# Optimization experiments

Hardware: AMD Instinct MI355X
Metric: run time of the kernel (lower is better)

## Reference

```python
import jax, jax.numpy as jnp
import numpy as np

B, T, D, L, VOCAB = 4, 2048, 512, 3, 256


def setup_inputs() -> dict:
    key = jax.random.key(0)
    ks = jax.random.split(key, 5)
    x = jax.random.randint(ks[0], (B, T), 0, VOCAB, dtype=jnp.int32)
    embed = jax.random.normal(ks[1], (VOCAB, D), dtype=jnp.float32) * 0.02
    k = jnp.ones((L,), dtype=jnp.float32)
    ln_gamma = jnp.ones((L, D), dtype=jnp.float32)
    ln_beta = jnp.zeros((L, D), dtype=jnp.float32)
    W1 = jax.random.normal(ks[2], (L, D, 4 * D), dtype=jnp.float32) * 0.02
    b1 = jnp.zeros((L, 4 * D), dtype=jnp.float32)
    W2 = jax.random.normal(ks[3], (L, 4 * D, D), dtype=jnp.float32) * 0.02
    b2 = jnp.zeros((L, D), dtype=jnp.float32)
    return {"x": x, "embed": embed, "k": k, "ln_gamma": ln_gamma,
            "ln_beta": ln_beta, "W1": W1, "b1": b1, "W2": W2, "b2": b2}


def _layernorm(x, g, b, eps=1e-3):  # keras default eps=1e-3
    mu = jnp.mean(x, axis=-1, keepdims=True)
    var = jnp.mean(jnp.square(x - mu), axis=-1, keepdims=True)
    return (x - mu) * jax.lax.rsqrt(var + eps) * g + b


def reference(x, embed, k, ln_gamma, ln_beta, W1, b1, W2, b2):
    h = embed[x]  # (B,T,D)
    # CumprodBoundaryDimension: cumprod over feature dim, tanh, cumsum over time
    bd = jnp.cumsum(jnp.tanh(jnp.cumprod(h, axis=-1)), axis=1)
    h = h + h * bd
    t = jnp.arange(T)
    dist = jnp.abs((t[:, None] - t[None, :]).astype(jnp.float32))  # (T,T)
    causal = (t[None, :] <= t[:, None]).astype(jnp.float32)
    for l in range(L):
        # DeltaImportance
        h_cum = jnp.cumsum(h, axis=1)
        h_prev = jnp.pad(h[:, :-1, :], ((0, 0), (1, 0), (0, 0)))
        mag = jnp.linalg.norm(h_cum - h_prev, axis=-1)  # (B,T)
        decay = jnp.exp(-jax.nn.softplus(k[l]) * dist) * causal  # (T,T)
        # importance[b,i,j] = mag[b,i]*decay[i,j]; context = importance @ h
        ctx = jnp.abs(mag[:, :, None] * jnp.einsum('ij,bjd->bid', decay, h))
        y = _layernorm(ctx, ln_gamma[l], ln_beta[l])
        y = jax.nn.gelu(y @ W1[l] + b1[l], approximate=False) @ W2[l] + b2[l]
        h = h + y
    return h @ embed.T  # tied output projection (B,T,VOCAB)
```

## Files before the change

### kernel.cpp

```cpp
#include <hip/hip_runtime.h>
#include <math.h>


constexpr int Bc = 4, Tc = 2048, Dc = 512, Hc = 2048, Vc = 256;
constexpr int TSF = 16, NCF = 128;

typedef __attribute__((ext_vector_type(8))) short short8;
typedef __attribute__((ext_vector_type(4))) float f32x4;

__device__ inline unsigned short f2bf(float f) {
  unsigned int u = __float_as_uint(f);
  u += 0x7fffu + ((u >> 16) & 1u);
  return (unsigned short)(u >> 16);
}

__device__ inline void gload_lds16(const void* g, void* l) {
  __builtin_amdgcn_global_load_lds(
      (const __attribute__((address_space(1))) void*)g,
      (__attribute__((address_space(3))) void*)l, 16, 0, 0);
}

__device__ inline void wvm_dyn(int n) {
  switch (n) {
    case 14: asm volatile("s_waitcnt vmcnt(14)" ::: "memory"); break;
    case 12: asm volatile("s_waitcnt vmcnt(12)" ::: "memory"); break;
    case 10: asm volatile("s_waitcnt vmcnt(10)" ::: "memory"); break;
    case 8:  asm volatile("s_waitcnt vmcnt(8)"  ::: "memory"); break;
    case 6:  asm volatile("s_waitcnt vmcnt(6)"  ::: "memory"); break;
    case 4:  asm volatile("s_waitcnt vmcnt(4)"  ::: "memory"); break;
    case 2:  asm volatile("s_waitcnt vmcnt(2)"  ::: "memory"); break;
    default: asm volatile("s_waitcnt vmcnt(0)"  ::: "memory"); break;
  }
}
__device__ inline void barrier_raw() {
  asm volatile("s_barrier" ::: "memory");
}

__device__ inline float gelu_f(float z) {
  float x = z * 0.707106781186547524f;
  float ax = fabsf(x);
  float t = __builtin_amdgcn_rcpf(fmaf(0.3275911f, ax, 1.0f));
  float poly = t*(0.254829592f + t*(-0.284496736f + t*(1.421413741f +
               t*(-1.453152027f + t*1.061405429f))));
  float er = 1.0f - poly * __expf(-ax*ax);
  er = copysignf(er, x);
  return 0.5f * z * (1.0f + er);
}

__device__ inline float decay_w(const float* kvec, int l) {
  float kk = kvec[l];
  float sp = kk > 0.f ? kk + log1pf(expf(-kk)) : log1pf(expf(kk));
  return expf(-sp);
}

__device__ inline void tr32(const float* Wl, unsigned short* Wtl,
                            int R, int C, int c0, int r0, int tid,
                            float (*tile)[33]) {
  int tx = tid & 31, ty = tid >> 5;
  for (int i = ty; i < 32; i += 8)
    tile[i][tx] = Wl[(size_t)(r0+i)*C + (c0+tx)];
  __syncthreads();
  int rx = tid & 7, ry = tid >> 3;
  ushort4 o;
  o.x = f2bf(tile[rx*4+0][ry]);
  o.y = f2bf(tile[rx*4+1][ry]);
  o.z = f2bf(tile[rx*4+2][ry]);
  o.w = f2bf(tile[rx*4+3][ry]);
  *(ushort4*)&Wtl[(size_t)(c0+ry)*R + (r0 + rx*4)] = o;
}

__global__ __launch_bounds__(256) void wprep(
    const float* __restrict__ W1, unsigned short* __restrict__ W1t,
    const float* __restrict__ W2, unsigned short* __restrict__ W2t,
    const float* __restrict__ embed, unsigned short* __restrict__ emb)
{
  __shared__ float tile[32][33];
  int bid = blockIdx.x, tid = threadIdx.x;
  if (bid < 3072) {
    int l = bid >> 10, rem = bid & 1023;
    int cx = rem & 63, ry = rem >> 6;
    tr32(W1 + (size_t)l*Dc*Hc, W1t + (size_t)l*Dc*Hc, Dc, Hc,
         cx*32, ry*32, tid, tile);
  } else if (bid < 6144) {
    int b2 = bid - 3072;
    int l = b2 >> 10, rem = b2 & 1023;
    int cx = rem & 15, ry = rem >> 4;
    tr32(W2 + (size_t)l*Hc*Dc, W2t + (size_t)l*Hc*Dc, Hc, Dc,
         cx*32, ry*32, tid, tile);
  } else {
    int i = ((bid - 6144)*256 + tid) * 4;
    if (i < Vc*Dc) {
      float4 v = *(const float4*)&embed[i];
      ushort4 o;
      o.x = f2bf(v.x); o.y = f2bf(v.y); o.z = f2bf(v.z); o.w = f2bf(v.w);
      *(ushort4*)&emb[i] = o;
    }
  }
}

__global__ __launch_bounds__(1024) void embed_part(
    const int* __restrict__ x, const float* __restrict__ embed,
    float* __restrict__ th, float* __restrict__ partA)
{
  int c = blockIdx.x, b = blockIdx.y;
  int wv = threadIdx.x >> 6, lane = threadIdx.x & 63;
  int token = b*Tc + c*TSF + wv;
  int row = x[token];
  const float* e = embed + (size_t)row * Dc + lane * 8;
  float v[8];
  {
    float4 a = *(const float4*)e;
    float4 bb = *(const float4*)(e + 4);
    v[0]=a.x; v[1]=a.y; v[2]=a.z; v[3]=a.w;
    v[4]=bb.x; v[5]=bb.y; v[6]=bb.z; v[7]=bb.w;
  }
  float p = v[0];
  #pragma unroll
  for (int j=1;j<8;++j) p *= v[j];
  float incl = p;
  #pragma unroll
  for (int off=1; off<64; off<<=1) {
    float t = __shfl_up(incl, off);
    if (lane >= off) incl *= t;
  }
  float excl = __shfl_up(incl, 1);
  if (lane == 0) excl = 1.0f;
  float cc = excl;
  float o[8];
  #pragma unroll
  for (int j=0;j<8;++j) { cc *= v[j]; o[j] = tanhf(cc); }
  float* dst = th + (size_t)token * Dc + lane * 8;
  *(float4*)dst     = make_float4(o[0],o[1],o[2],o[3]);
  *(float4*)(dst+4) = make_float4(o[4],o[5],o[6],o[7]);
  __syncthreads();
  int d = threadIdx.x;
  if (d < Dc) {
    const float* pp = th + ((size_t)b*Tc + c*TSF)*Dc + d;
    float s = 0.f;
    #pragma unroll
    for (int t=0;t<TSF;++t) s += pp[(size_t)t*Dc];
    partA[((size_t)b*NCF + c)*Dc + d] = s;
  }
}

__global__ __launch_bounds__(512) void part_prefix(float* __restrict__ part)
{
  int pair = blockIdx.x * 8 + (threadIdx.x >> 6);
  int lane = threadIdx.x & 63;
  int b = pair >> 9, d = pair & 511;
  size_t i0 = ((size_t)b*NCF + 2*lane)*Dc + d;
  float v0 = part[i0];
  float v1 = part[i0 + Dc];
  float ps = v0 + v1;
  float incl = ps;
  #pragma unroll
  for (int off=1; off<64; off<<=1) {
    float t = __shfl_up(incl, off);
    if (lane >= off) incl += t;
  }
  float excl = incl - ps;
  part[i0]      = excl;
  part[i0 + Dc] = excl + v0;
}

__global__ __launch_bounds__(512) void bd_apply(
    const float* __restrict__ th, const float* __restrict__ partA,
    const int* __restrict__ x, const float* __restrict__ embed,
    float* __restrict__ h, float* __restrict__ partB,
    float* __restrict__ partW, const float* __restrict__ kvec)
{
  int c = blockIdx.x, b = blockIdx.y, d = threadIdx.x;
  float w0 = decay_w(kvec, 0);
  float acc = partA[((size_t)b*NCF + c)*Dc + d];
  float hsum = 0.f, psW = 0.f;
  #pragma unroll
  for (int t=0;t<TSF;++t) {
    int tt = c*TSF + t;
    size_t idx = ((size_t)b*Tc + tt)*Dc + d;
    acc += th[idx];
    int row = x[b*Tc + tt];
    float e = embed[(size_t)row*Dc + d];
    float hv = e * (1.0f + acc);
    h[idx] = hv;
    hsum += hv;
    psW = psW * w0 + hv;
  }
  partB[((size_t)b*NCF + c)*Dc + d] = hsum;
  partW[((size_t)b*NCF + c)*Dc + d] = psW;
}

__global__ __launch_bounds__(512) void mag_scan_ln(
    const float* __restrict__ h, const float* __restrict__ part,
    const float* __restrict__ partW,
    const float* __restrict__ kvec, int l,
    const float* __restrict__ g, const float* __restrict__ bt,
    unsigned short* __restrict__ yb)
{
  __shared__ float redA[8][TSF];
  __shared__ float redB[8][TSF];
  __shared__ float mag[TSF], muS[TSF], rsS[TSF];
  int c = blockIdx.x, b = blockIdx.y, d = threadIdx.x;
  int lane = d & 63, wv = d >> 6;
  float acc = part[((size_t)b*NCF + c)*Dc + d];
  int t0 = c * TSF;
  const float* hbase = h + (size_t)b*Tc*Dc + d;
  float hp = (t0 > 0) ? hbase[(size_t)(t0-1)*Dc] : 0.f;
  float hv[TSF];
  #pragma unroll
  for (int t=0;t<TSF;++t) {
    hv[t] = hbase[(size_t)(t0+t)*Dc];
    acc += hv[t];
    float diff = acc - hp;
    hp = hv[t];
    float s = diff * diff;
    #pragma unroll
    for (int off=32; off; off>>=1) s += __shfl_down(s, off);
    if (!lane) redA[wv][t] = s;
  }
  float w = decay_w(kvec, l);
  float s = (c > 0) ? partW[((size_t)b*NCF + (c-1))*Dc + d] : 0.f;
  __syncthreads();
  if (d < TSF) {
    float m = 0.f;
    #pragma unroll
    for (int w2=0;w2<8;++w2) m += redA[w2][d];
    mag[d] = sqrtf(m);
  }
  __syncthreads();
  #pragma unroll
  for (int t=0;t<TSF;++t) {
    s = hv[t] + w * s;
    float cv = mag[t] * fabsf(s);
    hv[t] = cv;
    float s1 = cv, s2 = cv * cv;
    #pragma unroll
    for (int off=32; off; off>>=1) {
      s1 += __shfl_down(s1, off);
      s2 += __shfl_down(s2, off);
    }
    if (!lane) { redA[wv][t] = s1; redB[wv][t] = s2; }
  }
  __syncthreads();
  if (d < TSF) {
    float m1 = 0.f, m2 = 0.f;
    #pragma unroll
    for (int w2=0;w2<8;++w2) { m1 += redA[w2][d]; m2 += redB[w2][d]; }
    float mu = m1 * (1.f/Dc);
    float var = fmaxf(m2 * (1.f/Dc) - mu*mu, 0.f);
    muS[d] = mu;
    rsS[d] = rsqrtf(var + 1e-3f);
  }
  __syncthreads();
  float gv = g[l*Dc + d], bv = bt[l*Dc + d];
  unsigned short* yp = yb + ((size_t)b*Tc + t0)*Dc + d;
  #pragma unroll
  for (int t=0;t<TSF;++t)
    yp[(size_t)t*Dc] = f2bf((hv[t] - muS[t]) * rsS[t] * gv + bv);
}

template<int CH> __device__ inline int swz(int row) {
  if constexpr (CH == 8) return row & 7;
  else return (row >> 1) & 3;
}

template<int EPI, int TM, int TN, int RING, int LEAD>
__global__ __launch_bounds__(512, 2) void mgemm8(
    const unsigned short* __restrict__ A,
    const unsigned short* __restrict__ Bt,
    const float* __restrict__ bias,
    float* __restrict__ C, unsigned short* __restrict__ Cb,
    float* __restrict__ part, float* __restrict__ partW,
    const float* __restrict__ kvec, int wl,
    int N, int K, int nrow)
{
  constexpr int BK = 32;
  constexpr int PA = TM/128, PB = TN/128;
  constexpr int LPT = PA + PB;
  constexpr int WM = TM/2, WN = TN/4;
  constexpr int AM = WM/16, AN = WN/16, AH = AM/2;
  constexpr int ASTG = TM*BK, BSTG = TN*BK;
  __shared__ unsigned short As[RING*ASTG];
  __shared__ unsigned short Bs[RING*BSTG];
  int tid = threadIdx.x;
  int lane = tid & 63, w = tid >> 6;
  int wr = w >> 2, wc = w & 3;
  int bid = blockIdx.x;
  int xcd = bid & 7, i = bid >> 3;
  int npx = nrow >> 3;
  int m0 = (xcd * npx + (i % npx)) * TM;
  int n0 = (i / npx) * TN;

  const unsigned short* ag[PA];
  const unsigned short* bg[PB];
  int aldst[PA], bldst[PB];
  #pragma unroll
  for (int p=0;p<PA;++p) {
    int ci = p*512 + tid;
    int row = ci >> 2, cp = ci & 3;
    int cg = cp ^ ((row >> 1) & 3);
    ag[p] = A + (size_t)(m0+row)*K + cg*8;
    aldst[p] = (p*512 + w*64)*8;
  }
  #pragma unroll
  for (int p=0;p<PB;++p) {
    int ci = p*512 + tid;
    int row = ci >> 2, cp = ci & 3;
    int cg = cp ^ ((row >> 1) & 3);
    bg[p] = Bt + (size_t)(n0+row)*K + cg*8;
    bldst[p] = (p*512 + w*64)*8;
  }

  int r = lane & 15, quad = lane >> 4;
  int sz = (quad ^ ((r >> 1) & 3)) * 8;
  int aoff[AM], boff[AN];
  #pragma unroll
  for (int fi=0; fi<AM; ++fi)
    aoff[fi] = (wr*WM + fi*16 + r)*BK + sz;
  #pragma unroll
  for (int fj=0; fj<AN; ++fj)
    boff[fj] = (wc*WN + fj*16 + r)*BK + sz;

  f32x4 acc[AM][AN];
  #pragma unroll
  for (int fi=0;fi<AM;++fi)
    #pragma unroll
    for (int fj=0;fj<AN;++fj)
      acc[fi][fj] = (f32x4){0.f,0.f,0.f,0.f};

  auto STAGE_A = [&](int t) {
    int kk = t * BK, sl = t & (RING-1);
    #pragma unroll
    for (int p=0;p<PA;++p) gload_lds16(ag[p] + kk, &As[sl*ASTG + aldst[p]]);
  };
  auto STAGE_B = [&](int t) {
    int kk = t * BK, sl = t & (RING-1);
    #pragma unroll
    for (int p=0;p<PB;++p) gload_lds16(bg[p] + kk, &Bs[sl*BSTG + bldst[p]]);
  };

  int nk = K / BK;
  #pragma unroll
  for (int t=0;t<LEAD;++t) {
    if (t < nk) { STAGE_A(t); STAGE_B(t); }
  }

  for (int kt = 0; kt < nk; ++kt) {
    int infl = nk - kt; if (infl > LEAD) infl = LEAD;
    wvm_dyn((infl - 1) * LPT);
    barrier_raw();
    int s = kt & (RING-1);
    short8 bfr[AN], af[AH];
    #pragma unroll
    for (int fj=0;fj<AN;++fj) bfr[fj] = *(const short8*)&Bs[s*BSTG + boff[fj]];
    #pragma unroll
    for (int fi=0;fi<AH;++fi) af[fi] = *(const short8*)&As[s*ASTG + aoff[fi]];
    if (kt + LEAD < nk) STAGE_A(kt + LEAD);
    __builtin_amdgcn_s_setprio(1);
    #pragma unroll
    for (int fi=0;fi<AH;++fi)
      #pragma unroll
      for (int fj=0;fj<AN;++fj)
        acc[fi][fj] = __builtin_amdgcn_mfma_f32_16x16x32_bf16(
            af[fi], bfr[fj], acc[fi][fj], 0, 0, 0);
    __builtin_amdgcn_s_setprio(0);
    barrier_raw();
    #pragma unroll
    for (int fi=0;fi<AH;++fi) af[fi] = *(const short8*)&As[s*ASTG + aoff[AH+fi]];
    if (kt + LEAD < nk) STAGE_B(kt + LEAD);
    __builtin_amdgcn_s_setprio(1);
    #pragma unroll
    for (int fi=0;fi<AH;++fi)
      #pragma unroll
      for (int fj=0;fj<AN;++fj)
        acc[AH+fi][fj] = __builtin_amdgcn_mfma_f32_16x16x32_bf16(
            af[fi], bfr[fj], acc[AH+fi][fj], 0, 0, 0);
    __builtin_amdgcn_s_setprio(0);
  }

  float wnext = 0.f, invw = 0.f, pwbase = 0.f;
  if (EPI == 1 && partW) {
    wnext = decay_w(kvec, wl);
    invw = 1.0f / wnext;
    pwbase = 1.0f;
    for (int q = 0; q < 15 - quad*4; ++q) pwbase *= wnext;
  }

  #pragma unroll
  for (int fi=0;fi<AM;++fi) {
    int rowb = m0 + wr*WM + fi*16 + quad*4;
    #pragma unroll
    for (int fj=0;fj<AN;++fj) {
      int col = n0 + wc*WN + fj*16 + r;
      float bv = bias[col];
      float ps = 0.f, psW = 0.f, pw = pwbase;
      #pragma unroll
      for (int reg=0;reg<4;++reg) {
        size_t idx = (size_t)(rowb + reg) * N + col;
        float z = acc[fi][fj][reg] + bv;
        if (EPI == 0) {
          Cb[idx] = f2bf(gelu_f(z));
        } else {
          float hv = C[idx] + z;
          C[idx] = hv;
          ps += hv;
          if (partW) { psW += pw * hv; pw *= invw; }
          if (Cb) Cb[idx] = f2bf(hv);
        }
      }
      if (EPI == 1 && part) {
        ps += __shfl_xor(ps, 16);
        ps += __shfl_xor(ps, 32);
        if (partW) {
          psW += __shfl_xor(psW, 16);
          psW += __shfl_xor(psW, 32);
        }
        if (quad == 0) {
          int chunk = (m0 + wr*WM + fi*16) >> 4;
          part[(size_t)chunk * N + col] = ps;
          if (partW) partW[(size_t)chunk * N + col] = psW;
        }
      }
    }
  }
}

template<int EPI, int TM, int TN, int BK>
__global__ __launch_bounds__(256) void mgemm(
    const unsigned short* __restrict__ A,
    const unsigned short* __restrict__ Bt,
    const float* __restrict__ bias,
    float* __restrict__ C, unsigned short* __restrict__ Cb,
    float* __restrict__ part, float* __restrict__ partW,
    const float* __restrict__ kvec, int wl,
    int N, int K, int nrow)
{
  constexpr int CH = BK / 8;
  constexpr int PA = TM*CH/256, PB = TN*CH/256;
  constexpr int WM = TM/2, WN = TN/2;
  constexpr int AM = WM/16, AN = WN/16;
  constexpr int NKH = BK/32;
  constexpr int ASTG = TM*BK, BSTG = TN*BK;
  __shared__ unsigned short As[2*ASTG];
  __shared__ unsigned short Bs[2*BSTG];
  int tid = threadIdx.x;
  int lane = tid & 63, w = tid >> 6;
  int wr = w >> 1, wc = w & 1;
  int bid = blockIdx.x;
  int xcd = bid & 7, i = bid >> 3;
  int npx = nrow >> 3;
  int m0 = (xcd * npx + (i % npx)) * TM;
  int n0 = (i / npx) * TN;

  const unsigned short* ag[PA];
  const unsigned short* bg[PB];
  int aldst[PA], bldst[PB];
  #pragma unroll
  for (int p=0;p<PA;++p) {
    int ci = p*256 + tid;
    int row = ci / CH, cp = ci % CH;
    int cg = cp ^ swz<CH>(row);
    ag[p] = A + (size_t)(m0+row)*K + cg*8;
    aldst[p] = (p*256 + w*64)*8;
  }
  #pragma unroll
  for (int p=0;p<PB;++p) {
    int ci = p*256 + tid;
    int row = ci / CH, cp = ci % CH;
    int cg = cp ^ swz<CH>(row);
    bg[p] = Bt + (size_t)(n0+row)*K + cg*8;
    bldst[p] = (p*256 + w*64)*8;
  }

  int r = lane & 15, quad = lane >> 4;
  int aoff[NKH][AM], boff[NKH][AN];
  #pragma unroll
  for (int kh=0;kh<NKH;++kh) {
    int cb = kh*4 + quad;
    #pragma unroll
    for (int i2=0;i2<AM;++i2)
      aoff[kh][i2] = (wr*WM + i2*16 + r)*BK + ((cb ^ swz<CH>(r)) & (CH-1))*8;
    #pragma unroll
    for (int j=0;j<AN;++j)
      boff[kh][j] = (wc*WN + j*16 + r)*BK + ((cb ^ swz<CH>(r)) & (CH-1))*8;
  }

  f32x4 acc[AM][AN];
  #pragma unroll
  for (int i2=0;i2<AM;++i2)
    #pragma unroll
    for (int j=0;j<AN;++j)
      acc[i2][j] = (f32x4){0.f,0.f,0.f,0.f};

  #pragma unroll
  for (int p=0;p<PA;++p) gload_lds16(ag[p], &As[aldst[p]]);
  #pragma unroll
  for (int p=0;p<PB;++p) gload_lds16(bg[p], &Bs[bldst[p]]);

  int nk = K / BK;
  for (int ki = 0; ki < nk; ++ki) {
    __syncthreads();
    int cur = ki & 1, nxt = cur ^ 1;
    if (ki + 1 < nk) {
      int kk = (ki + 1) * BK;
      #pragma unroll
      for (int p=0;p<PA;++p) gload_lds16(ag[p] + kk, &As[nxt*ASTG + aldst[p]]);
      #pragma unroll
      for (int p=0;p<PB;++p) gload_lds16(bg[p] + kk, &Bs[nxt*BSTG + bldst[p]]);
    }
    #pragma unroll
    for (int kh=0;kh<NKH;++kh) {
      short8 af[AM], bfr[AN];
      #pragma unroll
      for (int i2=0;i2<AM;++i2) af[i2] = *(const short8*)&As[cur*ASTG + aoff[kh][i2]];
      #pragma unroll
      for (int j=0;j<AN;++j) bfr[j] = *(const short8*)&Bs[cur*BSTG + boff[kh][j]];
      #pragma unroll
      for (int i2=0;i2<AM;++i2)
        #pragma unroll
        for (int j=0;j<AN;++j)
          acc[i2][j] = __builtin_amdgcn_mfma_f32_16x16x32_bf16(af[i2], bfr[j], acc[i2][j], 0, 0, 0);
    }
  }

  #pragma unroll
  for (int i2=0;i2<AM;++i2) {
    int rowb = m0 + wr*WM + i2*16 + quad*4;
    #pragma unroll
    for (int j=0;j<AN;++j) {
      int col = n0 + wc*WN + j*16 + r;
      #pragma unroll
      for (int reg=0;reg<4;++reg) {
        size_t idx = (size_t)(rowb + reg) * N + col;
        C[idx] = acc[i2][j][reg];
      }
    }
  }
}

extern "C" void kernel_launch(void* const* d_in, const int* in_sizes, int n_in,
                              void* d_out, int out_size, void* d_ws, size_t ws_size,
                              hipStream_t stream) {
  const int*   x     = (const int*)  d_in[0];
  const float* embed = (const float*)d_in[1];
  const float* kvec  = (const float*)d_in[2];
  const float* g     = (const float*)d_in[3];
  const float* bt    = (const float*)d_in[4];
  const float* W1    = (const float*)d_in[5];
  const float* b1    = (const float*)d_in[6];
  const float* W2    = (const float*)d_in[7];
  const float* b2    = (const float*)d_in[8];
  float* out = (float*)d_out;

  const size_t NTD = (size_t)Bc * Tc * Dc;
  const size_t NTH = (size_t)Bc * Tc * Hc;
  char* wsb = (char*)d_ws;
  float* h      = (float*)wsb;                wsb += NTD*4;
  float* tmpA   = (float*)wsb;                wsb += NTD*4;
  float* partA  = (float*)wsb;                wsb += (size_t)Bc*NCF*Dc*4;
  float* partB  = (float*)wsb;                wsb += (size_t)Bc*NCF*Dc*4;
  float* partW  = (float*)wsb;                wsb += (size_t)Bc*NCF*Dc*4;
  unsigned short* yb   = (unsigned short*)wsb; wsb += NTD*2;
  unsigned short* a1b  = (unsigned short*)wsb; wsb += NTH*2;
  unsigned short* hb   = (unsigned short*)wsb; wsb += NTD*2;
  unsigned short* W1t  = (unsigned short*)wsb; wsb += (size_t)3*Dc*Hc*2;
  unsigned short* W2t  = (unsigned short*)wsb; wsb += (size_t)3*Dc*Hc*2;
  unsigned short* emb  = (unsigned short*)wsb; wsb += (size_t)Vc*Dc*2;

  wprep<<<dim3(6144 + (Vc*Dc)/1024), 256, 0, stream>>>(
      W1, W1t, W2, W2t, embed, emb);

  embed_part<<<dim3(NCF, Bc), 1024, 0, stream>>>(x, embed, tmpA, partA);
  part_prefix<<<dim3(256), 512, 0, stream>>>(partA);
  bd_apply<<<dim3(NCF, Bc), 512, 0, stream>>>(tmpA, partA, x, embed, h,
                                              partB, partW, kvec);
  part_prefix<<<dim3(256), 512, 0, stream>>>(partB);

  for (int l = 0; l < 3; ++l) {
    mag_scan_ln<<<dim3(NCF, Bc), 512, 0, stream>>>(h, partB, partW, kvec, l,
                                                   g, bt, yb);
    mgemm8<0,256,256,4,3><<<dim3(256), 512, 0, stream>>>(
        yb, W1t + (size_t)l*Hc*Dc, b1 + (size_t)l*Hc, nullptr, a1b,
        nullptr, nullptr, kvec, 0, Hc, Dc, 32);
    mgemm8<1,128,128,8,7><<<dim3(256), 512, 0, stream>>>(
        a1b, W2t + (size_t)l*Dc*Hc, b2 + (size_t)l*Dc, h,
        (l == 2) ? hb : nullptr,
        (l < 2) ? partB : nullptr, (l < 2) ? partW : nullptr, kvec, l + 1,
        Dc, Hc, 64);
    if (l < 2) part_prefix<<<dim3(256), 512, 0, stream>>>(partB);
  }
  mgemm<2,64,64,32><<<dim3(128*(Vc/64)), 256, 0, stream>>>(
      hb, emb, nullptr, out, nullptr, nullptr, nullptr, kvec, 0,
      Vc, Dc, 128);
}
```

Measured before the change: 424.2 us.

## Use intra-block split-K with BK=64 for the second FFN GEMM

```diff
diff --git a/kernel.cpp b/kernel.cpp
--- a/kernel.cpp
+++ b/kernel.cpp
@@ -22,9 +22,7 @@
 
 __device__ inline void wvm_dyn(int n) {
   switch (n) {
-    case 14: asm volatile("s_waitcnt vmcnt(14)" ::: "memory"); break;
     case 12: asm volatile("s_waitcnt vmcnt(12)" ::: "memory"); break;
-    case 10: asm volatile("s_waitcnt vmcnt(10)" ::: "memory"); break;
     case 8:  asm volatile("s_waitcnt vmcnt(8)"  ::: "memory"); break;
     case 6:  asm volatile("s_waitcnt vmcnt(6)"  ::: "memory"); break;
     case 4:  asm volatile("s_waitcnt vmcnt(4)"  ::: "memory"); break;
@@ -269,7 +267,6 @@
     const unsigned short* __restrict__ Bt,
     const float* __restrict__ bias,
     float* __restrict__ C, unsigned short* __restrict__ Cb,
-    float* __restrict__ part, float* __restrict__ partW,
     const float* __restrict__ kvec, int wl,
     int N, int K, int nrow)
 {
@@ -377,14 +374,6 @@
     __builtin_amdgcn_s_setprio(0);
   }
 
-  float wnext = 0.f, invw = 0.f, pwbase = 0.f;
-  if (EPI == 1 && partW) {
-    wnext = decay_w(kvec, wl);
-    invw = 1.0f / wnext;
-    pwbase = 1.0f;
-    for (int q = 0; q < 15 - quad*4; ++q) pwbase *= wnext;
-  }
-
   #pragma unroll
   for (int fi=0;fi<AM;++fi) {
     int rowb = m0 + wr*WM + fi*16 + quad*4;
@@ -392,32 +381,186 @@
     for (int fj=0;fj<AN;++fj) {
       int col = n0 + wc*WN + fj*16 + r;
       float bv = bias[col];
-      float ps = 0.f, psW = 0.f, pw = pwbase;
       #pragma unroll
       for (int reg=0;reg<4;++reg) {
         size_t idx = (size_t)(rowb + reg) * N + col;
-        float z = acc[fi][fj][reg] + bv;
-        if (EPI == 0) {
-          Cb[idx] = f2bf(gelu_f(z));
-        } else {
-          float hv = C[idx] + z;
+        Cb[idx] = f2bf(gelu_f(acc[fi][fj][reg] + bv));
+      }
+    }
+  }
+}
+
+template<int EPI>
+__global__ __launch_bounds__(512, 1) void mgemm8k(
+    const unsigned short* __restrict__ A,
+    const unsigned short* __restrict__ Bt,
+    const float* __restrict__ bias,
+    float* __restrict__ C, unsigned short* __restrict__ Cb,
+    float* __restrict__ part, float* __restrict__ partW,
+    const float* __restrict__ kvec, int wl,
+    int N, int K, int nrow)
+{
+  constexpr int TM = 128, TN = 128, BKF = 64;
+  constexpr int PA = 2, PB = 2, LPT = 4;
+  constexpr int RING = 4, LEAD = 3;
+  constexpr int ASTG = TM*BKF, BSTG = TN*BKF;
+  __shared__ unsigned short As[RING*ASTG];
+  __shared__ unsigned short Bs[RING*BSTG];
+  int tid = threadIdx.x;
+  int lane = tid & 63, w = tid >> 6;
+  int wr = w >> 2, wc = (w >> 1) & 1, ks = w & 1;
+  int bid = blockIdx.x;
+  int xcd = bid & 7, i = bid >> 3;
+  int npx = nrow >> 3;
+  int m0 = (xcd * npx + (i % npx)) * TM;
+  int n0 = (i / npx) * TN;
+
+  const unsigned short* ag[PA];
+  const unsigned short* bg[PB];
+  int aldst[PA], bldst[PB];
+  #pragma unroll
+  for (int p=0;p<PA;++p) {
+    int ci = p*512 + tid;
+    int row = ci >> 3, cp = ci & 7;
+    int cg = cp ^ (row & 7);
+    ag[p] = A + (size_t)(m0+row)*K + cg*8;
+    aldst[p] = (p*512 + w*64)*8;
+  }
+  #pragma unroll
+  for (int p=0;p<PB;++p) {
+    int ci = p*512 + tid;
+    int row = ci >> 3, cp = ci & 7;
+    int cg = cp ^ (row & 7);
+    bg[p] = Bt + (size_t)(n0+row)*K + cg*8;
+    bldst[p] = (p*512 + w*64)*8;
+  }
+
+  int r = lane & 15, quad = lane >> 4;
+  int cb = ks*4 + quad;
+  int aoff[4], boff[4];
+  #pragma unroll
+  for (int fi=0; fi<4; ++fi)
+    aoff[fi] = (wr*64 + fi*16 + r)*BKF + ((cb ^ (r & 7)) & 7)*8;
+  #pragma unroll
+  for (int fj=0; fj<4; ++fj)
+    boff[fj] = (wc*64 + fj*16 + r)*BKF + ((cb ^ (r & 7)) & 7)*8;
+
+  f32x4 acc[4][4];
+  #pragma unroll
+  for (int fi=0;fi<4;++fi)
+    #pragma unroll
+    for (int fj=0;fj<4;++fj)
+      acc[fi][fj] = (f32x4){0.f,0.f,0.f,0.f};
+
+  auto STAGE_A = [&](int t) {
+    int kk = t * BKF, sl = t & (RING-1);
+    #pragma unroll
+    for (int p=0;p<PA;++p) gload_lds16(ag[p] + kk, &As[sl*ASTG + aldst[p]]);
+  };
+  auto STAGE_B = [&](int t) {
+    int kk = t * BKF, sl = t & (RING-1);
+    #pragma unroll
+    for (int p=0;p<PB;++p) gload_lds16(bg[p] + kk, &Bs[sl*BSTG + bldst[p]]);
+  };
+
+  int nk = K / BKF;
+  STAGE_A(0); STAGE_B(0);
+  STAGE_A(1); STAGE_B(1);
+  STAGE_A(2); STAGE_B(2);
+
+  for (int kt = 0; kt < nk; ++kt) {
+    int infl = nk - kt; if (infl > LEAD) infl = LEAD;
+    wvm_dyn((infl - 1) * LPT);
+    barrier_raw();
+    int s = kt & (RING-1);
+    short8 bfr[4], af[2];
+    #pragma unroll
+    for (int fj=0;fj<4;++fj) bfr[fj] = *(const short8*)&Bs[s*BSTG + boff[fj]];
+    #pragma unroll
+    for (int fi=0;fi<2;++fi) af[fi] = *(const short8*)&As[s*ASTG + aoff[fi]];
+    if (kt + LEAD < nk) STAGE_A(kt + LEAD);
+    __builtin_amdgcn_s_setprio(1);
+    #pragma unroll
+    for (int fi=0;fi<2;++fi)
+      #pragma unroll
+      for (int fj=0;fj<4;++fj)
+        acc[fi][fj] = __builtin_amdgcn_mfma_f32_16x16x32_bf16(
+            af[fi], bfr[fj], acc[fi][fj], 0, 0, 0);
+    __builtin_amdgcn_s_setprio(0);
+    barrier_raw();
+    #pragma unroll
+    for (int fi=0;fi<2;++fi) af[fi] = *(const short8*)&As[s*ASTG + aoff[2+fi]];
+    if (kt + LEAD < nk) STAGE_B(kt + LEAD);
+    __builtin_amdgcn_s_setprio(1);
+    #pragma unroll
+    for (int fi=0;fi<2;++fi)
+      #pragma unroll
+      for (int fj=0;fj<4;++fj)
+        acc[2+fi][fj] = __builtin_amdgcn_mfma_f32_16x16x32_bf16(
+            af[fi], bfr[fj], acc[2+fi][fj], 0, 0, 0);
+    __builtin_amdgcn_s_setprio(0);
+  }
+
+  __syncthreads();
+  float4* scr4 = (float4*)As;
+  int pidx = wr*2 + wc;
+  float4* base = scr4 + pidx*1024 + lane*16;
+  if (ks == 1) {
+    #pragma unroll
+    for (int p=0;p<16;++p) {
+      int slot = (p + lane) & 15;
+      int fi = p >> 2, fj = p & 3;
+      base[slot] = make_float4(acc[fi][fj][0], acc[fi][fj][1],
+                               acc[fi][fj][2], acc[fi][fj][3]);
+    }
+  }
+  __syncthreads();
+  if (ks == 0) {
+    #pragma unroll
+    for (int p=0;p<16;++p) {
+      int slot = (p + lane) & 15;
+      int fi = p >> 2, fj = p & 3;
+      float4 v = base[slot];
+      acc[fi][fj][0] += v.x; acc[fi][fj][1] += v.y;
+      acc[fi][fj][2] += v.z; acc[fi][fj][3] += v.w;
+    }
+
+    float wnext = 0.f, invw = 0.f, pwbase = 0.f;
+    if (EPI == 1 && partW) {
+      wnext = decay_w(kvec, wl);
+      invw = 1.0f / wnext;
+      pwbase = 1.0f;
+      for (int q = 0; q < 15 - quad*4; ++q) pwbase *= wnext;
+    }
+    #pragma unroll
+    for (int fi=0;fi<4;++fi) {
+      int rowb = m0 + wr*64 + fi*16 + quad*4;
+      #pragma unroll
+      for (int fj=0;fj<4;++fj) {
+        int col = n0 + wc*64 + fj*16 + r;
+        float bv = bias[col];
+        float ps = 0.f, psW = 0.f, pw = pwbase;
+        #pragma unroll
+        for (int reg=0;reg<4;++reg) {
+          size_t idx = (size_t)(rowb + reg) * N + col;
+          float hv = C[idx] + acc[fi][fj][reg] + bv;
           C[idx] = hv;
           ps += hv;
           if (partW) { psW += pw * hv; pw *= invw; }
           if (Cb) Cb[idx] = f2bf(hv);
         }
-      }
-      if (EPI == 1 && part) {
-        ps += __shfl_xor(ps, 16);
-        ps += __shfl_xor(ps, 32);
-        if (partW) {
-          psW += __shfl_xor(psW, 16);
-          psW += __shfl_xor(psW, 32);
-        }
-        if (quad == 0) {
-          int chunk = (m0 + wr*WM + fi*16) >> 4;
-          part[(size_t)chunk * N + col] = ps;
-          if (partW) partW[(size_t)chunk * N + col] = psW;
+        if (part) {
+          ps += __shfl_xor(ps, 16);
+          ps += __shfl_xor(ps, 32);
+          if (partW) {
+            psW += __shfl_xor(psW, 16);
+            psW += __shfl_xor(psW, 32);
+          }
+          if (quad == 0) {
+            int chunk = (m0 + wr*64 + fi*16) >> 4;
+            part[(size_t)chunk * N + col] = ps;
+            if (partW) partW[(size_t)chunk * N + col] = psW;
+          }
         }
       }
     }
@@ -580,8 +723,8 @@
                                                    g, bt, yb);
     mgemm8<0,256,256,4,3><<<dim3(256), 512, 0, stream>>>(
         yb, W1t + (size_t)l*Hc*Dc, b1 + (size_t)l*Hc, nullptr, a1b,
-        nullptr, nullptr, kvec, 0, Hc, Dc, 32);
-    mgemm8<1,128,128,8,7><<<dim3(256), 512, 0, stream>>>(
+        kvec, 0, Hc, Dc, 32);
+    mgemm8k<1><<<dim3(256), 512, 0, stream>>>(
         a1b, W2t + (size_t)l*Dc*Hc, b2 + (size_t)l*Dc, h,
         (l == 2) ? hb : nullptr,
         (l < 2) ? partB : nullptr, (l < 2) ? partW : nullptr, kvec, l + 1,
```

New measurement: 416.2 us. Within noise of the previous version (-1.9%).
